# Kernel optimization log

Hardware: AMD Instinct MI355X
Metric: run time of the kernel (lower is better)

The kernel has to match this reference:

```python
import jax, jax.numpy as jnp
import numpy as np

VOCAB = 32000
WDIM = 768      # bert-base hidden size, per self.w_dim
H = 512         # lstm_hidden
NUM_CAT = 5
START = 3       # l2ind['SOS']
END = 4         # l2ind['EOS']
T = 2048
NEG = -10000.0


def _lstm_dir(x, Wih, Whh, bih, bhh, reverse):
    # x: [T, WDIM]; torch LSTM gate order: i, f, g, o
    z_in = x @ Wih.T + bih + bhh  # [T, 4H] precompute input projection
    def step(carry, zt):
        h, c = carry
        z = zt + h @ Whh.T
        i, f, g, o = jnp.split(z, 4)
        c = jax.nn.sigmoid(f) * c + jax.nn.sigmoid(i) * jnp.tanh(g)
        h = jax.nn.sigmoid(o) * jnp.tanh(c)
        return (h, c), h
    init = (jnp.zeros((H,), x.dtype), jnp.zeros((H,), x.dtype))
    _, hs = jax.lax.scan(step, init, z_in, reverse=reverse)
    return hs  # [T, H], aligned with input order


def setup_inputs():
    key = jax.random.key(0)
    ks = jax.random.split(key, 13)
    s = 0.05
    sent = jax.random.randint(ks[0], (T,), 0, VOCAB)
    emb = jax.random.normal(ks[1], (VOCAB, WDIM), jnp.float32) * 0.02
    Wih_f = jax.random.normal(ks[2], (4 * H, WDIM), jnp.float32) * s
    Whh_f = jax.random.normal(ks[3], (4 * H, H), jnp.float32) * s
    bih_f = jax.random.normal(ks[4], (4 * H,), jnp.float32) * s
    bhh_f = jax.random.normal(ks[5], (4 * H,), jnp.float32) * s
    Wih_b = jax.random.normal(ks[6], (4 * H, WDIM), jnp.float32) * s
    Whh_b = jax.random.normal(ks[7], (4 * H, H), jnp.float32) * s
    bih_b = jax.random.normal(ks[8], (4 * H,), jnp.float32) * s
    bhh_b = jax.random.normal(ks[9], (4 * H,), jnp.float32) * s
    fc_w = jax.random.normal(ks[10], (NUM_CAT, 2 * H), jnp.float32) * s
    fc_b = jax.random.normal(ks[11], (NUM_CAT,), jnp.float32) * s
    transitions = jax.random.normal(ks[12], (NUM_CAT, NUM_CAT), jnp.float32)
    transitions = transitions.at[START, :].set(NEG).at[:, END].set(NEG)
    return {"sent": sent, "emb": emb,
            "Wih_f": Wih_f, "Whh_f": Whh_f, "bih_f": bih_f, "bhh_f": bhh_f,
            "Wih_b": Wih_b, "Whh_b": Whh_b, "bih_b": bih_b, "bhh_b": bhh_b,
            "fc_w": fc_w, "fc_b": fc_b, "transitions": transitions}


def reference(sent, emb, Wih_f, Whh_f, bih_f, bhh_f, Wih_b, Whh_b, bih_b, bhh_b, fc_w, fc_b, transitions):
    # _get_scores: embedding -> BiLSTM -> fc
    x = emb[sent]                                   # [T, WDIM]
    h_f = _lstm_dir(x, Wih_f, Whh_f, bih_f, bhh_f, reverse=False)
    h_b = _lstm_dir(x, Wih_b, Whh_b, bih_b, bhh_b, reverse=True)
    out = jnp.concatenate([h_f, h_b], axis=-1)      # [T, 2H]
    feats = out @ fc_w.T + fc_b                     # [T, NUM_CAT]

    # _viterbi_decode: transitions[i, j] = score of moving from tag j to tag i
    init = feats[0] + transitions[:, START]         # [NUM_CAT]
    def vstep(layer, feat_t):
        # scores[i, j] = feat_t[i] + transitions[i, j] + layer[j]
        scores = feat_t[:, None] + transitions + layer[None, :]
        return jnp.max(scores, axis=1), jnp.argmax(scores, axis=1)
    layer, parents = jax.lax.scan(vstep, init, feats[1:])  # parents: [T-1, NUM_CAT]

    final = layer + transitions[END]
    idx0 = jnp.argmax(final)
    path_score = jnp.max(final)

    # backtrack (parents[0] of the original loop is all-START and gets popped)
    def btrack(idx, p):
        nxt = p[idx]
        return nxt, nxt
    _, idxs = jax.lax.scan(btrack, idx0, parents, reverse=True)  # [T-1]
    path = jnp.concatenate([idxs, idx0[None]])      # [T]
    return path, path_score
```

## Files before the change

### kernel.cpp

```cpp
#include <hip/hip_runtime.h>

#define TT 2048
#define WD 768
#define HH 512
#define G4 2048
#define NC 5
#define SENT 0xFFFFFFFFu

typedef float f4 __attribute__((ext_vector_type(4)));
typedef unsigned int u4 __attribute__((ext_vector_type(4)));

__global__ __launch_bounds__(256, 1) void fused_main(
    const int* __restrict__ sent, const float* __restrict__ emb,
    const float* __restrict__ Wih_f, const float* __restrict__ bih_f, const float* __restrict__ bhh_f,
    const float* __restrict__ Wih_b, const float* __restrict__ bih_b, const float* __restrict__ bhh_b,
    const float* __restrict__ Whh_f, const float* __restrict__ Whh_b,
    float* __restrict__ zin_f, float* __restrict__ zin_b,
    unsigned int* __restrict__ hw_f, unsigned int* __restrict__ hw_b,
    unsigned int* __restrict__ zcnt,
    const float* __restrict__ fc_w, const float* __restrict__ fc_b,
    float* __restrict__ feats)
{
    __shared__ float As[16][128];
    __shared__ float Bs[16][128];
    __shared__ float hs[HH];
    __shared__ float zb[256];

    const int tid = threadIdx.x;

    if (blockIdx.x >= 64) {
        const int lin  = blockIdx.x - 64;
        const int pair = lin >> 5;
        const int sub  = lin & 31;
        const int dirn = sub & 1;
        const int gx   = sub >> 1;
        const int ty   = dirn ? (15 - pair) : pair;

        const float* Wih = dirn ? Wih_b : Wih_f;
        const float* bih = dirn ? bih_b : bih_f;
        const float* bhh = dirn ? bhh_b : bhh_f;
        float* zin = dirn ? zin_b : zin_f;

        const int t0 = ty * 128;
        const int g0 = gx * 128;
        const int tm = tid >> 4, tn = tid & 15;

        float acc[8][8];
#pragma unroll
        for (int a = 0; a < 8; a++)
#pragma unroll
            for (int b = 0; b < 8; b++) acc[a][b] = 0.f;

        for (int kt = 0; kt < 48; ++kt) {
            const int k0 = kt * 16;
#pragma unroll
            for (int u = 0; u < 2; ++u) {
                const int s = tid * 2 + u;
                const int m = s >> 2, kq = s & 3;
                const int rowA = sent[t0 + m];
                float4 av = *(const float4*)(emb + (size_t)rowA * WD + k0 + kq * 4);
                As[kq * 4 + 0][m] = av.x; As[kq * 4 + 1][m] = av.y;
                As[kq * 4 + 2][m] = av.z; As[kq * 4 + 3][m] = av.w;
                float4 bv = *(const float4*)(Wih + (size_t)(g0 + m) * WD + k0 + kq * 4);
                Bs[kq * 4 + 0][m] = bv.x; Bs[kq * 4 + 1][m] = bv.y;
                Bs[kq * 4 + 2][m] = bv.z; Bs[kq * 4 + 3][m] = bv.w;
            }
            __syncthreads();
#pragma unroll
            for (int kk = 0; kk < 16; ++kk) {
                float4 a0 = *(const float4*)&As[kk][tm * 8];
                float4 a1 = *(const float4*)&As[kk][tm * 8 + 4];
                float4 b0 = *(const float4*)&Bs[kk][tn * 8];
                float4 b1 = *(const float4*)&Bs[kk][tn * 8 + 4];
                float av8[8] = {a0.x, a0.y, a0.z, a0.w, a1.x, a1.y, a1.z, a1.w};
                float bv8[8] = {b0.x, b0.y, b0.z, b0.w, b1.x, b1.y, b1.z, b1.w};
#pragma unroll
                for (int a = 0; a < 8; a++)
#pragma unroll
                    for (int b = 0; b < 8; b++) acc[a][b] += av8[a] * bv8[b];
            }
            __syncthreads();
        }
        float bias[8];
#pragma unroll
        for (int b = 0; b < 8; b++) { int g = g0 + tn * 8 + b; bias[b] = bih[g] + bhh[g]; }
#pragma unroll
        for (int a = 0; a < 8; a++) {
            const int t = t0 + tm * 8 + a;
            float* op = zin + (size_t)t * G4 + g0 + tn * 8;
            f4 o0 = {acc[a][0] + bias[0], acc[a][1] + bias[1], acc[a][2] + bias[2], acc[a][3] + bias[3]};
            f4 o1 = {acc[a][4] + bias[4], acc[a][5] + bias[5], acc[a][6] + bias[6], acc[a][7] + bias[7]};
            asm volatile("global_store_dwordx4 %0, %1, off sc1" :: "v"(op), "v"(o0) : "memory");
            asm volatile("global_store_dwordx4 %0, %1, off sc1" :: "v"(op + 4), "v"(o1) : "memory");
        }
        __syncthreads();
        if (tid == 0) atomicAdd(&zcnt[dirn * 16 + ty], 1u);
        return;
    }

    const int bid = blockIdx.x;
    const int d = bid >> 5;
    const int k = bid & 31;
    const float* zin = d ? zin_b : zin_f;
    const float* Whh = d ? Whh_b : Whh_f;
    unsigned int* hw = d ? hw_b : hw_f;

    const int q = tid >> 6;
    const int r = tid & 63;
    const int gate = r >> 4, jj = r & 15;
    const int grow = gate * HH + k * 16 + jj;

    const f4* wp = (const f4*)(Whh + (size_t)grow * HH + q * 128);
    f4 w[32];
#pragma unroll
    for (int i = 0; i < 32; ++i) w[i] = wp[i];
#pragma unroll
    for (int i = 0; i < 32; ++i)
        asm volatile("" : "+a"(w[i]));

    float c = 0.f;
    const int l = tid;
    const int g = l >> 4, j = l & 15;
    const int n16 = k * 16 + j;

    int readyty = -1;

    for (int it = 0; it < TT; ++it) {
        const int t = d ? (TT - 1 - it) : it;

        float z = 0.f;
        if (tid < 64) {
            const int tyc = t >> 7;
            if (tyc != readyty) {
                const unsigned int* cp = zcnt + d * 16 + tyc;
                unsigned int cv;
                do {
                    asm volatile("global_load_dword %0, %1, off sc0 sc1\n\t"
                                 "s_waitcnt vmcnt(0)"
                                 : "=v"(cv) : "v"(cp) : "memory");
                } while (cv < 16u);
                readyty = tyc;
            }
            z = zin[(size_t)t * G4 + g * HH + n16];
        }

        if (it > 0 && tid < 64) {
            const int tp = d ? (t + 1) : (t - 1);
            const unsigned int* pa = hw + (size_t)tp * HH + l * 8;
            u4 a0, a1;
            for (;;) {
                asm volatile(
                    "global_load_dwordx4 %0, %2, off sc0 sc1\n\t"
                    "global_load_dwordx4 %1, %2, off offset:16 sc0 sc1\n\t"
                    "s_waitcnt vmcnt(0)"
                    : "=v"(a0), "=v"(a1) : "v"(pa) : "memory");
                if (a0.x != SENT && a0.y != SENT && a0.z != SENT && a0.w != SENT &&
                    a1.x != SENT && a1.y != SENT && a1.z != SENT && a1.w != SENT) break;
            }
            u4* hd = (u4*)(hs + l * 8);
            hd[0] = a0; hd[1] = a1;
        }
        __syncthreads();

#pragma unroll
        for (int i = 0; i < 32; ++i) asm volatile("" : "+a"(w[i]));

        float part = 0.f;
        if (it > 0) {
            const f4* hv = ((const f4*)hs) + (q << 5);
#pragma unroll
            for (int i = 0; i < 32; ++i) {
                f4 h4 = hv[i];
                part += w[i].x * h4.x + w[i].y * h4.y + w[i].z * h4.z + w[i].w * h4.w;
            }
        }
        zb[tid] = part;
        __syncthreads();

        if (tid < 64) {
            float s = zb[l] + zb[64 + l] + zb[128 + l] + zb[192 + l];
            const float pre = z + s;
            float act;
            if (g == 2) act = tanhf(pre);
            else        act = 1.f / (1.f + expf(-pre));
            const float gi = __shfl(act, j);
            const float gf = __shfl(act, j + 16);
            const float gg = __shfl(act, j + 32);
            const float go = __shfl(act, j + 48);
            if (l < 16) {
                c = gf * c + gi * gg;
                const float hval = go * tanhf(c);
                __hip_atomic_store(&hw[(size_t)t * HH + k * 16 + l],
                                   __float_as_uint(hval),
                                   __ATOMIC_RELAXED, __HIP_MEMORY_SCOPE_AGENT);
            }
        }
    }

    {
        const int wgid = d * 32 + k;
        float* const rowbuf = (q < 2) ? (&As[0][0] + q * 1024)
                                      : (&Bs[0][0] + (q - 2) * 1024);
        for (int n = 0; n < 8; ++n) {
            const int t = (wgid * 4 + q) * 8 + n;
            {
                const unsigned int* pa = hw_f + (size_t)t * HH + r * 8;
                u4 a0, a1;
                for (;;) {
                    asm volatile(
                        "global_load_dwordx4 %0, %2, off sc0 sc1\n\t"
                        "global_load_dwordx4 %1, %2, off offset:16 sc0 sc1\n\t"
                        "s_waitcnt vmcnt(0)"
                        : "=v"(a0), "=v"(a1) : "v"(pa) : "memory");
                    if (a0.x != SENT && a0.y != SENT && a0.z != SENT && a0.w != SENT &&
                        a1.x != SENT && a1.y != SENT && a1.z != SENT && a1.w != SENT) break;
                }
                u4* dstp = (u4*)(rowbuf + r * 8);
                dstp[0] = a0; dstp[1] = a1;
            }
            {
                const unsigned int* pa = hw_b + (size_t)t * HH + r * 8;
                u4 a0, a1;
                for (;;) {
                    asm volatile(
                        "global_load_dwordx4 %0, %2, off sc0 sc1\n\t"
                        "global_load_dwordx4 %1, %2, off offset:16 sc0 sc1\n\t"
                        "s_waitcnt vmcnt(0)"
                        : "=v"(a0), "=v"(a1) : "v"(pa) : "memory");
                    if (a0.x != SENT && a0.y != SENT && a0.z != SENT && a0.w != SENT &&
                        a1.x != SENT && a1.y != SENT && a1.z != SENT && a1.w != SENT) break;
                }
                u4* dstp = (u4*)(rowbuf + HH + r * 8);
                dstp[0] = a0; dstp[1] = a1;
            }
            float facc[NC] = {0.f, 0.f, 0.f, 0.f, 0.f};
            for (int m = 0; m < 16; ++m) {
                const int cg = r + m * 64;
                const float hv = rowbuf[cg];
#pragma unroll
                for (int i = 0; i < NC; i++) facc[i] += hv * fc_w[i * (2 * HH) + cg];
            }
#pragma unroll
            for (int i = 0; i < NC; i++) {
#pragma unroll
                for (int off = 32; off; off >>= 1) facc[i] += __shfl_xor(facc[i], off);
            }
            if (r == 0) {
#pragma unroll
                for (int i = 0; i < NC; i++) feats[(size_t)t * NC + i] = facc[i] + fc_b[i];
            }
        }
    }
}

__global__ void viterbi_kernel(const float* __restrict__ feats,
                               const float* __restrict__ trans,
                               float* __restrict__ out)
{
    __shared__ float fs[TT * NC];
    __shared__ int par[TT];
    __shared__ float pathv[TT];
    __shared__ unsigned int maps[64];
    __shared__ int bidx[64];
    const int tid = threadIdx.x;
    for (int i = tid; i < TT * NC; i += 64) fs[i] = feats[i];
    float tr[25];
#pragma unroll
    for (int i = 0; i < 25; i++) tr[i] = trans[i];
    __syncthreads();

    float layer[NC];
#pragma unroll
    for (int i = 0; i < NC; i++) layer[i] = fs[i] + tr[i * 5 + 3];

    float ftc[NC];
#pragma unroll
    for (int i = 0; i < NC; i++) ftc[i] = fs[1 * NC + i];

    for (int s = 0; s < TT - 1; ++s) {
        const int sp = (s + 2 < TT) ? (s + 2) : (TT - 1);
        float ftn[NC];
#pragma unroll
        for (int i = 0; i < NC; i++) ftn[i] = fs[sp * NC + i];

        float nl[NC]; int pk = 0;
#pragma unroll
        for (int i = 0; i < NC; i++) {
            float best = tr[i * 5 + 0] + layer[0]; int bj = 0;
#pragma unroll
            for (int jj = 1; jj < NC; jj++) {
                const float v = tr[i * 5 + jj] + layer[jj];
                if (v > best) { best = v; bj = jj; }
            }
            nl[i] = ftc[i] + best;
            pk |= bj << (3 * i);
        }
#pragma unroll
        for (int i = 0; i < NC; i++) { layer[i] = nl[i]; ftc[i] = ftn[i]; }
        if (tid == 0) par[s] = pk;
    }
    float best = layer[0] + tr[20]; int idx0 = 0;
#pragma unroll
    for (int jj = 1; jj < NC; jj++) {
        const float v = layer[jj] + tr[20 + jj];
        if (v > best) { best = v; idx0 = jj; }
    }
    __syncthreads();

    const int slo = tid * 32;
    const int shi0 = slo + 31;
    const int shi = (shi0 < TT - 1) ? shi0 : (TT - 2);
    int preg[32];
#pragma unroll
    for (int u = 0; u < 32; ++u) {
        int su = slo + u; if (su > TT - 2) su = TT - 2;
        preg[u] = par[su];
    }
    int m0 = 0, m1 = 1, m2 = 2, m3 = 3, m4 = 4;
    for (int s = shi; s >= slo; --s) {
        const int pv = preg[s - slo];
        m0 = (pv >> (3 * m0)) & 7;
        m1 = (pv >> (3 * m1)) & 7;
        m2 = (pv >> (3 * m2)) & 7;
        m3 = (pv >> (3 * m3)) & 7;
        m4 = (pv >> (3 * m4)) & 7;
    }
    maps[tid] = (unsigned)(m0 | (m1 << 3) | (m2 << 6) | (m3 << 9) | (m4 << 12));
    __syncthreads();
    if (tid == 0) {
        int e = idx0;
        for (int cc = 63; cc >= 0; --cc) {
            bidx[cc] = e;
            e = (int)((maps[cc] >> (3 * e)) & 7u);
        }
    }
    __syncthreads();
    {
        int e = bidx[tid];
        for (int s = shi; s >= slo; --s) {
            e = (preg[s - slo] >> (3 * e)) & 7;
            pathv[s] = (float)e;
        }
    }
    if (tid == 0) { pathv[TT - 1] = (float)idx0; out[TT] = best; }
    __syncthreads();
    for (int i = tid; i < TT; i += 64) out[i] = pathv[i];
}

extern "C" void kernel_launch(void* const* d_in, const int* in_sizes, int n_in,
                              void* d_out, int out_size, void* d_ws, size_t ws_size,
                              hipStream_t stream) {
    const int*   sent   = (const int*)d_in[0];
    const float* emb    = (const float*)d_in[1];
    const float* Wih_f  = (const float*)d_in[2];
    const float* Whh_f  = (const float*)d_in[3];
    const float* bih_f  = (const float*)d_in[4];
    const float* bhh_f  = (const float*)d_in[5];
    const float* Wih_b  = (const float*)d_in[6];
    const float* Whh_b  = (const float*)d_in[7];
    const float* bih_b  = (const float*)d_in[8];
    const float* bhh_b  = (const float*)d_in[9];
    const float* fc_w   = (const float*)d_in[10];
    const float* fc_b   = (const float*)d_in[11];
    const float* trans  = (const float*)d_in[12];
    float* out = (float*)d_out;

    char* ws = (char*)d_ws;
    float* zin_f = (float*)ws;
    float* zin_b = (float*)(ws + (size_t)16777216);
    unsigned int* hw_f = (unsigned int*)(ws + (size_t)33554432);
    unsigned int* hw_b = (unsigned int*)(ws + (size_t)37748736);
    float* feats = (float*)(ws + (size_t)41943040);
    unsigned int* zcnt = (unsigned int*)(ws + (size_t)42008576);

    hipMemsetAsync(hw_f, 0xFF, (size_t)8388608, stream);
    hipMemsetAsync(zcnt, 0, (size_t)128, stream);

    fused_main<<<576, 256, 0, stream>>>(sent, emb,
                                        Wih_f, bih_f, bhh_f,
                                        Wih_b, bih_b, bhh_b,
                                        Whh_f, Whh_b,
                                        zin_f, zin_b, hw_f, hw_b, zcnt,
                                        fc_w, fc_b, feats);

    viterbi_kernel<<<1, 64, 0, stream>>>(feats, trans, out);
}
```

Baseline: 4.729 ms.

## Place recurrent LSTM workgroups on shared XCCs and fuse Viterbi into main kernel

Workgroups read the XCC id from a hardware register and take dynamic roles so that each LSTM direction's 32 recurrent workgroups land on a single XCC. They also exchange hidden states through a second buffer written without the sc1 bit and polled with non-coherent loads, so the per-step handoff can stay in the XCC-local L2. If that fast path spins too long it falls back to the coherent buffer. The Viterbi decode moves into an extra workgroup of the same launch, which waits on a feats completion counter, removing the second kernel launch. The cost is a larger memset, an extra hidden-state store per step, and a more fragile placement protocol that relies on co-residency.

```diff
diff --git a/kernel.cpp b/kernel.cpp
--- a/kernel.cpp
+++ b/kernel.cpp
@@ -10,26 +10,56 @@
 typedef float f4 __attribute__((ext_vector_type(4)));
 typedef unsigned int u4 __attribute__((ext_vector_type(4)));
 
-__global__ __launch_bounds__(256, 1) void fused_main(
+__global__ __launch_bounds__(256, 2) void fused_all(
     const int* __restrict__ sent, const float* __restrict__ emb,
     const float* __restrict__ Wih_f, const float* __restrict__ bih_f, const float* __restrict__ bhh_f,
     const float* __restrict__ Wih_b, const float* __restrict__ bih_b, const float* __restrict__ bhh_b,
     const float* __restrict__ Whh_f, const float* __restrict__ Whh_b,
     float* __restrict__ zin_f, float* __restrict__ zin_b,
     unsigned int* __restrict__ hw_f, unsigned int* __restrict__ hw_b,
-    unsigned int* __restrict__ zcnt,
+    unsigned int* __restrict__ hwl_f, unsigned int* __restrict__ hwl_b,
+    unsigned int* __restrict__ zcnt, unsigned int* __restrict__ ctl,
     const float* __restrict__ fc_w, const float* __restrict__ fc_b,
-    float* __restrict__ feats)
+    float* __restrict__ feats, const float* __restrict__ trans,
+    float* __restrict__ out)
 {
-    __shared__ float As[16][128];
-    __shared__ float Bs[16][128];
-    __shared__ float hs[HH];
-    __shared__ float zb[256];
-
+    __shared__ __align__(16) char SMEM[45568];
+    __shared__ int s_role;
     const int tid = threadIdx.x;
 
-    if (blockIdx.x >= 64) {
-        const int lin  = blockIdx.x - 64;
+    if (tid == 0) {
+        unsigned int xcc;
+        asm volatile("s_getreg_b32 %0, hwreg(20, 0, 32)" : "=s"(xcc));
+        xcc &= 7u;
+        const unsigned int slot = atomicAdd(&ctl[xcc], 1u) + 1u;
+        const unsigned int grp = slot >> 5, lig = slot & 31u;
+        const unsigned int mytag = 0x40000000u | (xcc << 8) | grp;
+        if (lig == 31u) {
+            if (atomicCAS(&ctl[9], SENT, mytag) != SENT) {
+                const unsigned int c0v = __hip_atomic_load(&ctl[9],
+                        __ATOMIC_RELAXED, __HIP_MEMORY_SCOPE_AGENT);
+                if (((c0v >> 8) & 7u) != xcc)
+                    atomicCAS(&ctl[10], SENT, mytag);
+            }
+        }
+        unsigned int c0, c1;
+        do {
+            c0 = __hip_atomic_load(&ctl[9],  __ATOMIC_RELAXED, __HIP_MEMORY_SCOPE_AGENT);
+            c1 = __hip_atomic_load(&ctl[10], __ATOMIC_RELAXED, __HIP_MEMORY_SCOPE_AGENT);
+        } while (c0 == SENT || c1 == SENT);
+        int role;
+        if      (c0 == mytag) role = (int)lig;
+        else if (c1 == mytag) role = 32 + (int)lig;
+        else    role = 64 + (int)(atomicAdd(&ctl[11], 1u) + 1u);
+        s_role = role;
+    }
+    __syncthreads();
+    const int role = s_role;
+
+    if (role >= 64 && role < 576) {
+        float (*As)[128] = (float(*)[128])SMEM;
+        float (*Bs)[128] = (float(*)[128])(SMEM + 8192);
+        const int lin  = role - 64;
         const int pair = lin >> 5;
         const int sub  = lin & 31;
         const int dirn = sub & 1;
@@ -98,12 +128,121 @@
         return;
     }
 
-    const int bid = blockIdx.x;
-    const int d = bid >> 5;
-    const int k = bid & 31;
+    if (role == 576) {
+        float* fs = (float*)SMEM;
+        unsigned short* par = (unsigned short*)(SMEM + 40960);
+        unsigned int* maps = (unsigned int*)(SMEM + 45056);
+        int* bidx = (int*)(SMEM + 45312);
+
+        if (tid == 0) {
+            const unsigned int* fp = &ctl[12];
+            unsigned int cv;
+            do {
+                asm volatile("global_load_dword %0, %1, off sc0 sc1\n\t"
+                             "s_waitcnt vmcnt(0)" : "=v"(cv) : "v"(fp) : "memory");
+            } while (cv != 255u);
+        }
+        __syncthreads();
+        for (int mm = 0; mm < 10; ++mm) {
+            const float* sp2 = feats + tid * 40 + mm * 4;
+            f4 v;
+            asm volatile("global_load_dwordx4 %0, %1, off sc0 sc1\n\t"
+                         "s_waitcnt vmcnt(0)" : "=v"(v) : "v"(sp2) : "memory");
+            *(f4*)(fs + tid * 40 + mm * 4) = v;
+        }
+        __syncthreads();
+
+        float best = 0.f; int idx0 = 0;
+        if (tid < 64) {
+            float tr[25];
+#pragma unroll
+            for (int i = 0; i < 25; i++) tr[i] = trans[i];
+            float layer[NC];
+#pragma unroll
+            for (int i = 0; i < NC; i++) layer[i] = fs[i] + tr[i * 5 + 3];
+            float ftc[NC];
+#pragma unroll
+            for (int i = 0; i < NC; i++) ftc[i] = fs[1 * NC + i];
+            for (int s = 0; s < TT - 1; ++s) {
+                const int sp = (s + 2 < TT) ? (s + 2) : (TT - 1);
+                float ftn[NC];
+#pragma unroll
+                for (int i = 0; i < NC; i++) ftn[i] = fs[sp * NC + i];
+                float nl[NC]; int pk = 0;
+#pragma unroll
+                for (int i = 0; i < NC; i++) {
+                    float b2 = tr[i * 5 + 0] + layer[0]; int bj = 0;
+#pragma unroll
+                    for (int jj = 1; jj < NC; jj++) {
+                        const float v = tr[i * 5 + jj] + layer[jj];
+                        if (v > b2) { b2 = v; bj = jj; }
+                    }
+                    nl[i] = ftc[i] + b2;
+                    pk |= bj << (3 * i);
+                }
+#pragma unroll
+                for (int i = 0; i < NC; i++) { layer[i] = nl[i]; ftc[i] = ftn[i]; }
+                if (tid == 0) par[s] = (unsigned short)pk;
+            }
+            best = layer[0] + tr[20]; idx0 = 0;
+#pragma unroll
+            for (int jj = 1; jj < NC; jj++) {
+                const float v = layer[jj] + tr[20 + jj];
+                if (v > best) { best = v; idx0 = jj; }
+            }
+        }
+        __syncthreads();
+
+        int preg[32]; int slo = 0, shi = 0;
+        if (tid < 64) {
+            slo = tid * 32;
+            const int shi0 = slo + 31;
+            shi = (shi0 < TT - 1) ? shi0 : (TT - 2);
+#pragma unroll
+            for (int u = 0; u < 32; ++u) {
+                int su = slo + u; if (su > TT - 2) su = TT - 2;
+                preg[u] = (int)par[su];
+            }
+            int m0 = 0, m1 = 1, m2 = 2, m3 = 3, m4 = 4;
+            for (int s = shi; s >= slo; --s) {
+                const int pv = preg[s - slo];
+                m0 = (pv >> (3 * m0)) & 7;
+                m1 = (pv >> (3 * m1)) & 7;
+                m2 = (pv >> (3 * m2)) & 7;
+                m3 = (pv >> (3 * m3)) & 7;
+                m4 = (pv >> (3 * m4)) & 7;
+            }
+            maps[tid] = (unsigned)(m0 | (m1 << 3) | (m2 << 6) | (m3 << 9) | (m4 << 12));
+        }
+        __syncthreads();
+        if (tid == 0) {
+            int e = idx0;
+            for (int cc = 63; cc >= 0; --cc) {
+                bidx[cc] = e;
+                e = (int)((maps[cc] >> (3 * e)) & 7u);
+            }
+        }
+        __syncthreads();
+        if (tid < 64) {
+            int e = bidx[tid];
+            for (int s = shi; s >= slo; --s) {
+                e = (preg[s - slo] >> (3 * e)) & 7;
+                out[s] = (float)e;
+            }
+        }
+        if (tid == 0) { out[TT - 1] = (float)idx0; out[TT] = best; }
+        return;
+    }
+    if (role > 576) return;
+
+    float* hs = (float*)SMEM;
+    float* zb = (float*)(SMEM + 2048);
+    const int d = role >> 5;
+    const int k = role & 31;
     const float* zin = d ? zin_b : zin_f;
     const float* Whh = d ? Whh_b : Whh_f;
-    unsigned int* hw = d ? hw_b : hw_f;
+    unsigned int* hw  = d ? hw_b  : hw_f;
+    unsigned int* hwl = d ? hwl_b : hwl_f;
 
     const int q = tid >> 6;
     const int r = tid & 63;
@@ -124,6 +263,10 @@
     const int n16 = k * 16 + j;
 
     int readyty = -1;
+    int fastok = 1;
+
+#define OK8 (a0.x != SENT && a0.y != SENT && a0.z != SENT && a0.w != SENT && \
+             a1.x != SENT && a1.y != SENT && a1.z != SENT && a1.w != SENT)
 
     for (int it = 0; it < TT; ++it) {
         const int t = d ? (TT - 1 - it) : it;
@@ -146,16 +289,31 @@
 
         if (it > 0 && tid < 64) {
             const int tp = d ? (t + 1) : (t - 1);
-            const unsigned int* pa = hw + (size_t)tp * HH + l * 8;
+            const unsigned int* pa = hw  + (size_t)tp * HH + l * 8;
             u4 a0, a1;
-            for (;;) {
-                asm volatile(
-                    "global_load_dwordx4 %0, %2, off sc0 sc1\n\t"
-                    "global_load_dwordx4 %1, %2, off offset:16 sc0 sc1\n\t"
-                    "s_waitcnt vmcnt(0)"
-                    : "=v"(a0), "=v"(a1) : "v"(pa) : "memory");
-                if (a0.x != SENT && a0.y != SENT && a0.z != SENT && a0.w != SENT &&
-                    a1.x != SENT && a1.y != SENT && a1.z != SENT && a1.w != SENT) break;
+            bool got = false;
+            if (fastok && it > 4) {
+                const unsigned int* pl = hwl + (size_t)tp * HH + l * 8;
+                int spins = 0;
+                for (;;) {
+                    asm volatile(
+                        "global_load_dwordx4 %0, %2, off sc0 nt\n\t"
+                        "global_load_dwordx4 %1, %2, off offset:16 sc0 nt\n\t"
+                        "s_waitcnt vmcnt(0)"
+                        : "=v"(a0), "=v"(a1) : "v"(pl) : "memory");
+                    if (OK8) { got = true; break; }
+                    if (++spins > 24) { fastok = 0; break; }
+                }
+            }
+            if (!got) {
+                for (;;) {
+                    asm volatile(
+                        "global_load_dwordx4 %0, %2, off sc0 sc1\n\t"
+                        "global_load_dwordx4 %1, %2, off offset:16 sc0 sc1\n\t"
+                        "s_waitcnt vmcnt(0)"
+                        : "=v"(a0), "=v"(a1) : "v"(pa) : "memory");
+                    if (OK8) break;
+                }
             }
             u4* hd = (u4*)(hs + l * 8);
             hd[0] = a0; hd[1] = a1;
@@ -190,17 +348,21 @@
             if (l < 16) {
                 c = gf * c + gi * gg;
                 const float hval = go * tanhf(c);
-                __hip_atomic_store(&hw[(size_t)t * HH + k * 16 + l],
-                                   __float_as_uint(hval),
-                                   __ATOMIC_RELAXED, __HIP_MEMORY_SCOPE_AGENT);
+                const unsigned int hvbits = __float_as_uint(hval);
+                unsigned int* hp  = &hw [(size_t)t * HH + k * 16 + l];
+                unsigned int* hlp = &hwl[(size_t)t * HH + k * 16 + l];
+                asm volatile(
+                    "global_store_dword %0, %2, off\n\t"
+                    "global_store_dword %1, %2, off sc1"
+                    :: "v"(hlp), "v"(hp), "v"(hvbits) : "memory");
             }
         }
     }
+#undef OK8
 
     {
         const int wgid = d * 32 + k;
-        float* const rowbuf = (q < 2) ? (&As[0][0] + q * 1024)
-                                      : (&Bs[0][0] + (q - 2) * 1024);
+        float* const rowbuf = (float*)(SMEM + 3072) + q * 1024;
         for (int n = 0; n < 8; ++n) {
             const int t = (wgid * 4 + q) * 8 + n;
             {
@@ -247,104 +409,17 @@
             }
             if (r == 0) {
 #pragma unroll
-                for (int i = 0; i < NC; i++) feats[(size_t)t * NC + i] = facc[i] + fc_b[i];
-            }
-        }
+                for (int i = 0; i < NC; i++) {
+                    const float fv = facc[i] + fc_b[i];
+                    float* fp2 = feats + (size_t)t * NC + i;
+                    asm volatile("global_store_dword %0, %1, off sc1"
+                                 :: "v"(fp2), "v"(fv) : "memory");
+                }
+            }
+        }
+        asm volatile("s_waitcnt vmcnt(0)" ::: "memory");
+        if (r == 0) atomicAdd(&ctl[12], 1u);
     }
-}
-
-__global__ void viterbi_kernel(const float* __restrict__ feats,
-                               const float* __restrict__ trans,
-                               float* __restrict__ out)
-{
-    __shared__ float fs[TT * NC];
-    __shared__ int par[TT];
-    __shared__ float pathv[TT];
-    __shared__ unsigned int maps[64];
-    __shared__ int bidx[64];
-    const int tid = threadIdx.x;
-    for (int i = tid; i < TT * NC; i += 64) fs[i] = feats[i];
-    float tr[25];
-#pragma unroll
-    for (int i = 0; i < 25; i++) tr[i] = trans[i];
-    __syncthreads();
-
-    float layer[NC];
-#pragma unroll
-    for (int i = 0; i < NC; i++) layer[i] = fs[i] + tr[i * 5 + 3];
-
-    float ftc[NC];
-#pragma unroll
-    for (int i = 0; i < NC; i++) ftc[i] = fs[1 * NC + i];
-
-    for (int s = 0; s < TT - 1; ++s) {
-        const int sp = (s + 2 < TT) ? (s + 2) : (TT - 1);
-        float ftn[NC];
-#pragma unroll
-        for (int i = 0; i < NC; i++) ftn[i] = fs[sp * NC + i];
-
-        float nl[NC]; int pk = 0;
-#pragma unroll
-        for (int i = 0; i < NC; i++) {
-            float best = tr[i * 5 + 0] + layer[0]; int bj = 0;
-#pragma unroll
-            for (int jj = 1; jj < NC; jj++) {
-                const float v = tr[i * 5 + jj] + layer[jj];
-                if (v > best) { best = v; bj = jj; }
-            }
-            nl[i] = ftc[i] + best;
-            pk |= bj << (3 * i);
-        }
-#pragma unroll
-        for (int i = 0; i < NC; i++) { layer[i] = nl[i]; ftc[i] = ftn[i]; }
-        if (tid == 0) par[s] = pk;
-    }
-    float best = layer[0] + tr[20]; int idx0 = 0;
-#pragma unroll
-    for (int jj = 1; jj < NC; jj++) {
-        const float v = layer[jj] + tr[20 + jj];
-        if (v > best) { best = v; idx0 = jj; }
-    }
-    __syncthreads();
-
-    const int slo = tid * 32;
-    const int shi0 = slo + 31;
-    const int shi = (shi0 < TT - 1) ? shi0 : (TT - 2);
-    int preg[32];
-#pragma unroll
-    for (int u = 0; u < 32; ++u) {
-        int su = slo + u; if (su > TT - 2) su = TT - 2;
-        preg[u] = par[su];
-    }
-    int m0 = 0, m1 = 1, m2 = 2, m3 = 3, m4 = 4;
-    for (int s = shi; s >= slo; --s) {
-        const int pv = preg[s - slo];
-        m0 = (pv >> (3 * m0)) & 7;
-        m1 = (pv >> (3 * m1)) & 7;
-        m2 = (pv >> (3 * m2)) & 7;
-        m3 = (pv >> (3 * m3)) & 7;
-        m4 = (pv >> (3 * m4)) & 7;
-    }
-    maps[tid] = (unsigned)(m0 | (m1 << 3) | (m2 << 6) | (m3 << 9) | (m4 << 12));
-    __syncthreads();
-    if (tid == 0) {
-        int e = idx0;
-        for (int cc = 63; cc >= 0; --cc) {
-            bidx[cc] = e;
-            e = (int)((maps[cc] >> (3 * e)) & 7u);
-        }
-    }
-    __syncthreads();
-    {
-        int e = bidx[tid];
-        for (int s = shi; s >= slo; --s) {
-            e = (preg[s - slo] >> (3 * e)) & 7;
-            pathv[s] = (float)e;
-        }
-    }
-    if (tid == 0) { pathv[TT - 1] = (float)idx0; out[TT] = best; }
-    __syncthreads();
-    for (int i = tid; i < TT; i += 64) out[i] = pathv[i];
 }
 
 extern "C" void kernel_launch(void* const* d_in, const int* in_sizes, int n_in,
@@ -368,20 +443,22 @@
     char* ws = (char*)d_ws;
     float* zin_f = (float*)ws;
     float* zin_b = (float*)(ws + (size_t)16777216);
-    unsigned int* hw_f = (unsigned int*)(ws + (size_t)33554432);
-    unsigned int* hw_b = (unsigned int*)(ws + (size_t)37748736);
-    float* feats = (float*)(ws + (size_t)41943040);
-    unsigned int* zcnt = (unsigned int*)(ws + (size_t)42008576);
-
-    hipMemsetAsync(hw_f, 0xFF, (size_t)8388608, stream);
+    unsigned int* hw_f  = (unsigned int*)(ws + (size_t)33554432);
+    unsigned int* hw_b  = (unsigned int*)(ws + (size_t)37748736);
+    unsigned int* hwl_f = (unsigned int*)(ws + (size_t)41943040);
+    unsigned int* hwl_b = (unsigned int*)(ws + (size_t)46137344);
+    float* feats = (float*)(ws + (size_t)50331648);
+    unsigned int* zcnt = (unsigned int*)(ws + (size_t)50397184);
+    unsigned int* ctl  = (unsigned int*)(ws + (size_t)50397312);
+
+    hipMemsetAsync(hw_f, 0xFF, (size_t)16777216, stream);
     hipMemsetAsync(zcnt, 0, (size_t)128, stream);
-
-    fused_main<<<576, 256, 0, stream>>>(sent, emb,
-                                        Wih_f, bih_f, bhh_f,
-                                        Wih_b, bih_b, bhh_b,
-                                        Whh_f, Whh_b,
-                                        zin_f, zin_b, hw_f, hw_b, zcnt,
-                                        fc_w, fc_b, feats);
-
-    viterbi_kernel<<<1, 64, 0, stream>>>(feats, trans, out);
+    hipMemsetAsync(ctl, 0xFF, (size_t)128, stream);
+
+    fused_all<<<577, 256, 0, stream>>>(sent, emb,
+                                       Wih_f, bih_f, bhh_f,
+                                       Wih_b, bih_b, bhh_b,
+                                       Whh_f, Whh_b,
+                                       zin_f, zin_b, hw_f, hw_b, hwl_f, hwl_b,
+                                       zcnt, ctl, fc_w, fc_b, feats, trans, out);
 }
```

Result: slower. 12.56 ms (+165.6%).
